# Kernel optimization log

Hardware: AMD Instinct MI355X
Metric: run time of the kernel (lower is better)

The kernel has to match this reference:

```python
import jax, jax.numpy as jnp
import numpy as np

B, S, D, H = 4, 2048, 1024, 16
DK = D // H


def setup_inputs() -> dict:
    key = jax.random.key(0)
    ks = jax.random.split(key, 5)
    init_std = np.sqrt(2.0 / (D + D))  # trunc bound proxy; plain randn clamped below
    trunc = 3 * init_std

    def w(k):
        return jnp.clip(jax.random.normal(k, (D, D), dtype=jnp.float32), -trunc, trunc)

    x = jax.random.normal(ks[0], (B, S, D), dtype=jnp.float32)
    return {
        "x": x,
        "W_Q": w(ks[1]),
        "W_K": w(ks[2]),
        "W_V": w(ks[3]),
        "W_O": w(ks[4]),
        "is_causal": 1,
    }


def reference(x, W_Q, W_K, W_V, W_O, is_causal):
    b, s, d = x.shape
    # Linear: y = W @ x with W:[out,in], x:[..., in]
    def proj(W, t):
        y = jnp.einsum("oi,bsi->bso", W, t)
        # [b, s, h*dk] -> [b, h, s, dk]
        return y.reshape(b, s, H, DK).transpose(0, 2, 1, 3)

    q = proj(W_Q, x)
    k = proj(W_K, x)
    v = proj(W_V, x)

    scores = jnp.einsum("bhqd,bhkd->bhqk", q, k) * (DK ** -0.5)
    if is_causal:
        causal = jnp.tril(jnp.ones((s, s), dtype=bool))
        scores = jnp.where(causal, scores, -jnp.inf)
    attn = jax.nn.softmax(scores, axis=-1)
    out = jnp.einsum("bhqk,bhkd->bhqd", attn, v)
    out = out.transpose(0, 2, 1, 3).reshape(b, s, H * DK)
    return jnp.einsum("oi,bsi->bso", W_O, out)
```

## Files before the change

kernel.cpp:

```cpp
#include <hip/hip_runtime.h>
#include <stdint.h>

#define NB 4
#define NS 2048
#define ND 1024
#define NH 16
#define NDK 64
#define L2E 1.44269504088896340736f
#define AS1 __attribute__((address_space(1)))
#define AS3 __attribute__((address_space(3)))

typedef __attribute__((ext_vector_type(8)))  short     s16x8;
typedef __attribute__((ext_vector_type(4)))  float     f32x4;
typedef __attribute__((ext_vector_type(16))) float     f32x16;
typedef __attribute__((ext_vector_type(4)))  unsigned  u32x4;

__device__ __forceinline__ unsigned short f2bf(float f) {
    union { float f; unsigned u; } v; v.f = f;
    unsigned r = v.u + 0x7FFFu + ((v.u >> 16) & 1u);
    return (unsigned short)(r >> 16);
}
__device__ __forceinline__ unsigned cvt_pk_bf16(float lo, float hi) {
    unsigned r;
    asm("v_cvt_pk_bf16_f32 %0, %1, %2" : "=v"(r) : "v"(lo), "v"(hi));
    return r;
}
__device__ __forceinline__ void pl32swap(unsigned &a, unsigned &b) {
    asm volatile("v_permlane32_swap_b32 %0, %1" : "+v"(a), "+v"(b));
}
__device__ __forceinline__ float exp2_hw(float x) {
    float r; asm("v_exp_f32 %0, %1" : "=v"(r) : "v"(x)); return r;
}
__device__ __forceinline__ f32x16 fz16() {
    f32x16 z;
#pragma unroll
    for (int r = 0; r < 16; ++r) z[r] = 0.f;
    return z;
}
__device__ __forceinline__ f32x16 mfma32(const s16x8& a, const s16x8& b, const f32x16& c) {
    return __builtin_amdgcn_mfma_f32_32x32x16_bf16(a, b, c, 0, 0, 0);
}

__global__ void detect_dtype(const unsigned* __restrict__ x, int* __restrict__ flag) {
    int lane = threadIdx.x;
    int cnt = 0;
    for (int i = lane; i < 1024; i += 64) {
        unsigned lo = x[i] & 0xFFFFu;
        unsigned e  = (lo >> 7) & 0xFFu;
        cnt += (e >= 100u && e <= 140u) ? 1 : 0;
    }
    for (int d = 1; d < 64; d <<= 1) cnt += __shfl_xor(cnt, d);
    if (lane == 0) flag[0] = (cnt > 512) ? 1 : 0;
}

__global__ void convert_bf16(const void* __restrict__ src, unsigned short* __restrict__ dst,
                             int n8, const int* __restrict__ flagp) {
    int i = blockIdx.x * blockDim.x + threadIdx.x;
    int stride = gridDim.x * blockDim.x;
    int fl = *flagp;
    for (; i < n8; i += stride) {
        u32x4 v;
        if (fl) {
            v = *(const u32x4*)((const unsigned short*)src + (long)i * 8);
        } else {
            const float* p = (const float*)src + (long)i * 8;
            f32x4 a = *(const f32x4*)p;
            f32x4 b = *(const f32x4*)(p + 4);
            v[0] = cvt_pk_bf16(a[0], a[1]);
            v[1] = cvt_pk_bf16(a[2], a[3]);
            v[2] = cvt_pk_bf16(b[0], b[1]);
            v[3] = cvt_pk_bf16(b[2], b[3]);
        }
        *(u32x4*)(dst + (long)i * 8) = v;
    }
}

__device__ __forceinline__ void stage_glds64(const unsigned short* __restrict__ src, int ld,
                                             long r0, int k0, unsigned short* lds, int tid) {
#pragma unroll
    for (int h = 0; h < 4; ++h) {
        int c = h * 256 + tid;
        int row = c >> 3;
        int scol = (c & 7) ^ (row & 7);
        const unsigned short* gp = src + (r0 + row) * ld + k0 + scol * 8;
        unsigned short* lp = lds + (c & ~63) * 8;
        __builtin_amdgcn_global_load_lds(
            (const AS1 unsigned short*)gp, (AS3 unsigned short*)lp, 16, 0, 0);
    }
}
__device__ __forceinline__ void stage_orig64(unsigned short* lds, const void* __restrict__ src,
                                             int ld, long r0, int k0, int fl, int tid) {
    if (fl) { stage_glds64((const unsigned short*)src, ld, r0, k0, lds, tid); return; }
#pragma unroll
    for (int h = 0; h < 4; ++h) {
        int c = h * 256 + tid;
        int row = c >> 3;
        int scol = (c & 7) ^ (row & 7);
        const float* p = (const float*)src + (r0 + row) * (long)ld + k0 + scol * 8;
        f32x4 a = *(const f32x4*)p;
        f32x4 b = *(const f32x4*)(p + 4);
        u32x4 v;
        v[0] = cvt_pk_bf16(a[0], a[1]);
        v[1] = cvt_pk_bf16(a[2], a[3]);
        v[2] = cvt_pk_bf16(b[0], b[1]);
        v[3] = cvt_pk_bf16(b[2], b[3]);
        *(u32x4*)(lds + c * 8) = v;
    }
}

template<int OUT_MODE, int A_ORIG, int B_ORIG, int GXL>
__global__ __launch_bounds__(256, 2)
void gemm3(const void* __restrict__ A, const void* __restrict__ W,
           void* __restrict__ dst, const int* __restrict__ flagp, float scale)
{
    __shared__ unsigned short As[128 * 64];
    __shared__ unsigned short Bs[128 * 64];
    const long TOKc = (long)NB * NS * ND;
    int tid  = threadIdx.x;
    int w    = tid >> 6, lane = tid & 63;
    int wr   = w >> 1,   wc   = w & 1;
    int nwg = (int)(gridDim.x * gridDim.y);
    int bid = (int)(blockIdx.y * gridDim.x + blockIdx.x);
    int nb  = (bid & 7) * (nwg >> 3) + (bid >> 3);
    int n0  = (nb & ((1 << GXL) - 1)) * 128;
    long m0 = (long)(nb >> GXL) * 128;
    int fl  = *flagp;

    f32x4 zero4 = {0.f, 0.f, 0.f, 0.f};
    f32x4 acc[4][4];
#pragma unroll
    for (int i = 0; i < 4; ++i)
#pragma unroll
        for (int j = 0; j < 4; ++j) acc[i][j] = zero4;

    int lr = lane & 15, lg = lane >> 4;

    for (int k0 = 0; k0 < 1024; k0 += 64) {
        __syncthreads();
        if (A_ORIG) stage_orig64(As, A, 1024, m0, k0, fl, tid);
        else        stage_glds64((const unsigned short*)A, 1024, m0, k0, As, tid);
        if (B_ORIG) stage_orig64(Bs, W, 1024, n0, k0, fl, tid);
        else        stage_glds64((const unsigned short*)W, 1024, n0, k0, Bs, tid);
        __syncthreads();
#pragma unroll
        for (int kk = 0; kk < 2; ++kk) {
            s16x8 af[4], bf[4];
#pragma unroll
            for (int i = 0; i < 4; ++i) {
                int row = wr * 64 + i * 16 + lr;
                int u = (kk * 4 + lg) ^ (lr & 7);
                af[i] = *(const s16x8*)(As + row * 64 + u * 8);
            }
#pragma unroll
            for (int j = 0; j < 4; ++j) {
                int row = wc * 64 + j * 16 + lr;
                int u = (kk * 4 + lg) ^ (lr & 7);
                bf[j] = *(const s16x8*)(Bs + row * 64 + u * 8);
            }
#pragma unroll
            for (int i = 0; i < 4; ++i)
#pragma unroll
                for (int j = 0; j < 4; ++j)
                    acc[i][j] = __builtin_amdgcn_mfma_f32_16x16x32_bf16(af[i], bf[j], acc[i][j], 0, 0, 0);
        }
    }

    int rbase = (lane >> 4) * 4;
#pragma unroll
    for (int i = 0; i < 4; ++i)
#pragma unroll
        for (int j = 0; j < 4; ++j)
#pragma unroll
            for (int r = 0; r < 4; ++r) {
                long m = m0 + wr * 64 + i * 16 + rbase + r;
                int  n = n0 + wc * 64 + j * 16 + lr;
                float v = acc[i][j][r];
                if (OUT_MODE == 0 || OUT_MODE == 3) {
                    long b = m >> 11, s = m & 2047;
                    int hh = (n >> 6) & 15, dk = n & 63;
                    float sc = (OUT_MODE == 0 || n < 1024) ? scale : 1.0f;
                    long off = (OUT_MODE == 3 && n >= 1024) ? TOKc : 0;
                    ((unsigned short*)dst)[off + (((b * NH + hh) * NS) + s) * NDK + dk] = f2bf(v * sc);
                } else if (OUT_MODE == 1) {
                    int hh = (int)(m >> 6), dk = (int)(m & 63);
                    long b = n >> 11, s = n & 2047;
                    ((unsigned short*)dst)[(((b * NH + hh) * NDK) + dk) * NS + s] = f2bf(v * scale);
                } else {
                    if (fl) ((unsigned short*)dst)[m * 1024 + n] = f2bf(v * scale);
                    else    ((float*)dst)[m * 1024 + n] = v * scale;
                }
            }
}

__device__ __forceinline__ void stage_tile64(const char* __restrict__ srcbase, int rowstride,
                                             unsigned short* lds, int tid) {
#pragma unroll
    for (int h = 0; h < 2; ++h) {
        int c = h * 256 + tid;
        int L = c * 16;
        int row = L >> 7;
        int sr  = (L & 127) ^ ((row & 7) << 4);
        const char* gp = srcbase + row * rowstride + sr;
        unsigned short* lp = lds + (c & ~63) * 8;
        __builtin_amdgcn_global_load_lds((const AS1 unsigned short*)gp,
                                         (AS3 unsigned short*)lp, 16, 0, 0);
    }
}

__device__ __forceinline__ void sm64s(f32x16& st0, f32x16& st1, float& l,
                                      bool mask, int kv0, int qb, int l31, int hi,
                                      s16x8* pf)
{
    if (mask) {
        int q = qb + l31;
#pragma unroll
        for (int r = 0; r < 16; ++r) {
            int crow = (r & 3) + 8 * (r >> 2) + 4 * hi;
            if (kv0 + crow > q)      st0[r] = -1e30f;
            if (kv0 + 32 + crow > q) st1[r] = -1e30f;
        }
    }
#pragma unroll
    for (int r = 0; r < 16; ++r) {
        st0[r] = exp2_hw(st0[r]);
        st1[r] = exp2_hw(st1[r]);
    }
    float s8[8];
#pragma unroll
    for (int r = 0; r < 8; ++r) s8[r] = (st0[r] + st0[r + 8]) + (st1[r] + st1[r + 8]);
    float s4[4];
#pragma unroll
    for (int r = 0; r < 4; ++r) s4[r] = s8[r] + s8[r + 4];
    l += (s4[0] + s4[1]) + (s4[2] + s4[3]);

#pragma unroll
    for (int half = 0; half < 2; ++half) {
        const f32x16& st = half ? st1 : st0;
        unsigned b0 = cvt_pk_bf16(st[0],  st[1]);
        unsigned b1 = cvt_pk_bf16(st[2],  st[3]);
        unsigned b2 = cvt_pk_bf16(st[4],  st[5]);
        unsigned b3 = cvt_pk_bf16(st[6],  st[7]);
        unsigned b4 = cvt_pk_bf16(st[8],  st[9]);
        unsigned b5 = cvt_pk_bf16(st[10], st[11]);
        unsigned b6 = cvt_pk_bf16(st[12], st[13]);
        unsigned b7 = cvt_pk_bf16(st[14], st[15]);
        pl32swap(b0, b2);  pl32swap(b1, b3);
        pl32swap(b4, b6);  pl32swap(b5, b7);
        union { unsigned u[4]; s16x8 v; } p0, p1;
        p0.u[0] = b0; p0.u[1] = b1; p0.u[2] = b2; p0.u[3] = b3;
        p1.u[0] = b4; p1.u[1] = b5; p1.u[2] = b6; p1.u[3] = b7;
        pf[half * 2]     = p0.v;
        pf[half * 2 + 1] = p1.v;
    }
}

__device__ __forceinline__ void attn_epi(unsigned short* epb, const f32x16& o0, const f32x16& o1,
                                         float lrow, int l31, int hi, int lane,
                                         unsigned short* __restrict__ Oo, int qb, int b, int hh)
{
    float lt = lrow + __shfl_xor(lrow, 32);
    float inv = 1.0f / lt;
#pragma unroll
    for (int j = 0; j < 2; ++j) {
        const f32x16& o = j ? o1 : o0;
#pragma unroll
        for (int g = 0; g < 4; ++g) {
            int d0 = j * 32 + g * 8 + hi * 4;
            unsigned lo = cvt_pk_bf16(o[g * 4 + 0] * inv, o[g * 4 + 1] * inv);
            unsigned hw = cvt_pk_bf16(o[g * 4 + 2] * inv, o[g * 4 + 3] * inv);
            unsigned short* p = epb + l31 * 72 + d0;
            *(unsigned*)(p)     = lo;
            *(unsigned*)(p + 2) = hw;
        }
    }
    asm volatile("s_waitcnt lgkmcnt(0)" ::: "memory");
    __builtin_amdgcn_sched_barrier(0);
#pragma unroll
    for (int rr = 0; rr < 4; ++rr) {
        int q2 = rr * 8 + (lane >> 3);
        int d2 = (lane & 7) * 8;
        u32x4 vv = *(const u32x4*)(epb + q2 * 72 + d2);
        *(u32x4*)(Oo + (((long)b * NS + qb + q2) * ND) + hh * NDK + d2) = vv;
    }
}

__global__ __launch_bounds__(256, 3)
void attn_fwd9(const unsigned short* __restrict__ Q,
               const unsigned short* __restrict__ Kt,
               const unsigned short* __restrict__ Vt,
               unsigned short* __restrict__ Oo,
               const int* __restrict__ causalp)
{
    __shared__ char lds[2][16384];
    int tid = threadIdx.x, w = tid >> 6, lane = tid & 63;
    int l31 = lane & 31, hi = lane >> 5;
    int bh = blockIdx.x;
    int j  = 15 - (int)blockIdx.y;
    int t  = 4 * j + w, qb = t * 32;
    int causal = *causalp;
    int nst   = causal ? (2 * j + 2) : (NS / 64);
    int sdiag = causal ? (t >> 1) : 0x7FFFFFFF;

    const unsigned short* Qh = Q  + bh * (NS * NDK);
    const char* Khb = (const char*)(Kt + (long)bh * NS * NDK);
    const char* Vhb = (const char*)(Vt + (long)bh * NDK * NS);

    s16x8 qf[4];
#pragma unroll
    for (int kd = 0; kd < 4; ++kd)
        qf[kd] = *(const s16x8*)(Qh + (qb + l31) * NDK + kd * 16 + hi * 8);

    int koff[4];
#pragma unroll
    for (int kd = 0; kd < 4; ++kd)
        koff[kd] = l31 * 128 + ((kd * 32 + hi * 16) ^ ((l31 & 7) << 4));

    const f32x16 Z16 = fz16();
    f32x16 o0 = fz16(), o1 = fz16();
    float l = 0.f;

    stage_tile64(Khb, 128, (unsigned short*)&lds[0][0], tid);
    stage_tile64(Vhb, NS * 2, (unsigned short*)&lds[0][8192], tid);
    __syncthreads();

    int cur = 0;
    for (int s = 0; s < nst; ++s) {
        if (s + 1 < nst) {
            int kv1 = (s + 1) * 64;
            stage_tile64(Khb + (long)kv1 * 128, 128, (unsigned short*)&lds[cur ^ 1][0], tid);
            stage_tile64(Vhb + kv1 * 2, NS * 2, (unsigned short*)&lds[cur ^ 1][8192], tid);
        }
        if (s <= sdiag) {
            const char* kb = &lds[cur][0];
            const char* vb = &lds[cur][8192];
            f32x16 st0, st1;
            {
                s16x8 k0 = *(const s16x8*)(kb + koff[0]);
                s16x8 k1 = *(const s16x8*)(kb + 4096 + koff[0]);
                st0 = mfma32(k0, qf[0], Z16);
                st1 = mfma32(k1, qf[0], Z16);
            }
#pragma unroll
            for (int kd = 1; kd < 4; ++kd) {
                s16x8 k0 = *(const s16x8*)(kb + koff[kd]);
                s16x8 k1 = *(const s16x8*)(kb + 4096 + koff[kd]);
                st0 = mfma32(k0, qf[kd], st0);
                st1 = mfma32(k1, qf[kd], st1);
            }
            s16x8 pf[4];
            sm64s(st0, st1, l, s == sdiag, s * 64, qb, l31, hi, pf);
#pragma unroll
            for (int ks = 0; ks < 4; ++ks) {
                s16x8 va = *(const s16x8*)(vb + koff[ks]);
                s16x8 wb = *(const s16x8*)(vb + 4096 + koff[ks]);
                o0 = mfma32(va, pf[ks], o0);
                o1 = mfma32(wb, pf[ks], o1);
            }
        }
        __syncthreads();
        cur ^= 1;
    }

    unsigned short* ep = (unsigned short*)&lds[0][0] + w * (32 * 72);
    attn_epi(ep, o0, o1, l, l31, hi, lane, Oo, qb, bh >> 4, bh & 15);
}

extern "C" void kernel_launch(void* const* d_in, const int* in_sizes, int n_in,
                              void* d_out, int out_size, void* d_ws, size_t ws_size,
                              hipStream_t stream) {
    const void* x  = d_in[0];
    const void* Wq = d_in[1];
    const void* Wk = d_in[2];
    const void* Wv = d_in[3];
    const void* Wo = d_in[4];
    const int* causal = (const int*)d_in[5];

    const long TOK  = (long)NB * NS * ND;
    const long WTOK = (long)ND * ND;
    size_t need = 256 + 4UL * TOK * 2;
    if (ws_size < need) return;

    char* ws = (char*)d_ws;
    int* flag = (int*)ws;
    unsigned short* Qb = (unsigned short*)(ws + 256);
    unsigned short* Kb = Qb + TOK;
    unsigned short* Vb = Kb + TOK;
    unsigned short* XB = Vb + TOK;
    unsigned short* Ab = XB;
    unsigned short* WQK = Vb + TOK - 2 * WTOK;
    unsigned short* WOB = Qb;

    detect_dtype<<<1, 64, 0, stream>>>((const unsigned*)x, flag);

    convert_bf16<<<2048, 256, 0, stream>>>(x,  XB,         (int)(TOK / 8),  flag);
    convert_bf16<<<512,  256, 0, stream>>>(Wq, WQK,        (int)(WTOK / 8), flag);
    convert_bf16<<<512,  256, 0, stream>>>(Wk, WQK + WTOK, (int)(WTOK / 8), flag);

    dim3 blk(256);
    gemm3<3, 0, 0, 4><<<dim3(16, 64), blk, 0, stream>>>(XB, WQK, Qb, flag, 0.125f * L2E);
    gemm3<1, 1, 0, 6><<<dim3(64, 8), blk, 0, stream>>>(Wv, XB, Vb, flag, 1.0f);
    attn_fwd9<<<dim3(64, 16), blk, 0, stream>>>(Qb, Kb, Vb, Ab, causal);
    convert_bf16<<<512, 256, 0, stream>>>(Wo, WOB, (int)(WTOK / 8), flag);
    gemm3<2, 0, 0, 3><<<dim3(8, 64), blk, 0, stream>>>(Ab, WOB, d_out, flag, 1.0f);
}
```

Measured before the change: 168.2 us.

## Balance causal attention tiles and pre-convert all QKV weights in one kernel

Merges the x, W_Q, W_K and W_V bf16 conversions into a single launch and stages W_V into scratch space at the tail of the output buffer. The V-projection GEMM then loads pre-converted bf16 through direct global-to-LDS loads instead of converting fp32 on the fly. The attention kernel now pairs a short and a long query tile per block (tiles 2j+w and 62-2j+w), so every block does a similar amount of causal work. The scratch area in d_out relies on the final GEMM overwriting it later, and the bf16-input path through the old stage_orig code has been removed.

```diff
diff --git a/kernel.cpp b/kernel.cpp
--- a/kernel.cpp
+++ b/kernel.cpp
@@ -51,6 +51,41 @@
     }
     for (int d = 1; d < 64; d <<= 1) cnt += __shfl_xor(cnt, d);
     if (lane == 0) flag[0] = (cnt > 512) ? 1 : 0;
+}
+
+__global__ void convert_all(const void* __restrict__ x,  const void* __restrict__ wq,
+                            const void* __restrict__ wk, const void* __restrict__ wv,
+                            unsigned short* __restrict__ XB, unsigned short* __restrict__ WQKV,
+                            const int* __restrict__ flagp) {
+    const int A  = (NB * NS * ND) / 8;
+    const int WC = (ND * ND) / 8;
+    int fl = *flagp;
+    int i = blockIdx.x * blockDim.x + threadIdx.x;
+    int stride = gridDim.x * blockDim.x;
+    int total = A + 3 * WC;
+    for (; i < total; i += stride) {
+        const void* src; unsigned short* dst; long o8;
+        if (i < A) { src = x; dst = XB; o8 = i; }
+        else {
+            int k = i - A, which = k >> 17, o = k & (WC - 1);
+            src = which == 0 ? wq : (which == 1 ? wk : wv);
+            dst = WQKV + (long)which * (ND * ND);
+            o8 = o;
+        }
+        u32x4 v;
+        if (fl) {
+            v = *(const u32x4*)((const unsigned short*)src + o8 * 8);
+        } else {
+            const float* p = (const float*)src + o8 * 8;
+            f32x4 a = *(const f32x4*)p;
+            f32x4 b = *(const f32x4*)(p + 4);
+            v[0] = cvt_pk_bf16(a[0], a[1]);
+            v[1] = cvt_pk_bf16(a[2], a[3]);
+            v[2] = cvt_pk_bf16(b[0], b[1]);
+            v[3] = cvt_pk_bf16(b[2], b[3]);
+        }
+        *(u32x4*)(dst + o8 * 8) = v;
+    }
 }
 
 __global__ void convert_bf16(const void* __restrict__ src, unsigned short* __restrict__ dst,
@@ -88,29 +123,10 @@
             (const AS1 unsigned short*)gp, (AS3 unsigned short*)lp, 16, 0, 0);
     }
 }
-__device__ __forceinline__ void stage_orig64(unsigned short* lds, const void* __restrict__ src,
-                                             int ld, long r0, int k0, int fl, int tid) {
-    if (fl) { stage_glds64((const unsigned short*)src, ld, r0, k0, lds, tid); return; }
-#pragma unroll
-    for (int h = 0; h < 4; ++h) {
-        int c = h * 256 + tid;
-        int row = c >> 3;
-        int scol = (c & 7) ^ (row & 7);
-        const float* p = (const float*)src + (r0 + row) * (long)ld + k0 + scol * 8;
-        f32x4 a = *(const f32x4*)p;
-        f32x4 b = *(const f32x4*)(p + 4);
-        u32x4 v;
-        v[0] = cvt_pk_bf16(a[0], a[1]);
-        v[1] = cvt_pk_bf16(a[2], a[3]);
-        v[2] = cvt_pk_bf16(b[0], b[1]);
-        v[3] = cvt_pk_bf16(b[2], b[3]);
-        *(u32x4*)(lds + c * 8) = v;
-    }
-}
-
-template<int OUT_MODE, int A_ORIG, int B_ORIG, int GXL>
+
+template<int OUT_MODE, int NXB>
 __global__ __launch_bounds__(256, 2)
-void gemm3(const void* __restrict__ A, const void* __restrict__ W,
+void gemm3(const unsigned short* __restrict__ A, const unsigned short* __restrict__ W,
            void* __restrict__ dst, const int* __restrict__ flagp, float scale)
 {
     __shared__ unsigned short As[128 * 64];
@@ -122,8 +138,8 @@
     int nwg = (int)(gridDim.x * gridDim.y);
     int bid = (int)(blockIdx.y * gridDim.x + blockIdx.x);
     int nb  = (bid & 7) * (nwg >> 3) + (bid >> 3);
-    int n0  = (nb & ((1 << GXL) - 1)) * 128;
-    long m0 = (long)(nb >> GXL) * 128;
+    int n0  = (nb % NXB) * 128;
+    long m0 = (long)(nb / NXB) * 128;
     int fl  = *flagp;
 
     f32x4 zero4 = {0.f, 0.f, 0.f, 0.f};
@@ -137,10 +153,8 @@
 
     for (int k0 = 0; k0 < 1024; k0 += 64) {
         __syncthreads();
-        if (A_ORIG) stage_orig64(As, A, 1024, m0, k0, fl, tid);
-        else        stage_glds64((const unsigned short*)A, 1024, m0, k0, As, tid);
-        if (B_ORIG) stage_orig64(Bs, W, 1024, n0, k0, fl, tid);
-        else        stage_glds64((const unsigned short*)W, 1024, n0, k0, Bs, tid);
+        stage_glds64(A, 1024, m0, k0, As, tid);
+        stage_glds64(W, 1024, n0, k0, Bs, tid);
         __syncthreads();
 #pragma unroll
         for (int kk = 0; kk < 2; ++kk) {
@@ -175,11 +189,11 @@
                 long m = m0 + wr * 64 + i * 16 + rbase + r;
                 int  n = n0 + wc * 64 + j * 16 + lr;
                 float v = acc[i][j][r];
-                if (OUT_MODE == 0 || OUT_MODE == 3) {
+                if (OUT_MODE == 3) {
                     long b = m >> 11, s = m & 2047;
                     int hh = (n >> 6) & 15, dk = n & 63;
-                    float sc = (OUT_MODE == 0 || n < 1024) ? scale : 1.0f;
-                    long off = (OUT_MODE == 3 && n >= 1024) ? TOKc : 0;
+                    float sc = (n < 1024) ? scale : 1.0f;
+                    long off = (n >= 1024) ? TOKc : 0;
                     ((unsigned short*)dst)[off + (((b * NH + hh) * NS) + s) * NDK + dk] = f2bf(v * sc);
                 } else if (OUT_MODE == 1) {
                     int hh = (int)(m >> 6), dk = (int)(m & 63);
@@ -285,20 +299,21 @@
 }
 
 __global__ __launch_bounds__(256, 3)
-void attn_fwd9(const unsigned short* __restrict__ Q,
-               const unsigned short* __restrict__ Kt,
-               const unsigned short* __restrict__ Vt,
-               unsigned short* __restrict__ Oo,
-               const int* __restrict__ causalp)
+void attn_fwd10(const unsigned short* __restrict__ Q,
+                const unsigned short* __restrict__ Kt,
+                const unsigned short* __restrict__ Vt,
+                unsigned short* __restrict__ Oo,
+                const int* __restrict__ causalp)
 {
     __shared__ char lds[2][16384];
     int tid = threadIdx.x, w = tid >> 6, lane = tid & 63;
     int l31 = lane & 31, hi = lane >> 5;
     int bh = blockIdx.x;
-    int j  = 15 - (int)blockIdx.y;
-    int t  = 4 * j + w, qb = t * 32;
+    int j  = blockIdx.y;
+    int t  = (w < 2) ? (2 * j + w) : (62 - 2 * j + (w & 1));
+    int qb = t * 32;
     int causal = *causalp;
-    int nst   = causal ? (2 * j + 2) : (NS / 64);
+    int nst   = causal ? (32 - j) : (NS / 64);
     int sdiag = causal ? (t >> 1) : 0x7FFFFFFF;
 
     const unsigned short* Qh = Q  + bh * (NS * NDK);
@@ -387,19 +402,16 @@
     unsigned short* Vb = Kb + TOK;
     unsigned short* XB = Vb + TOK;
     unsigned short* Ab = XB;
-    unsigned short* WQK = Vb + TOK - 2 * WTOK;
     unsigned short* WOB = Qb;
+    unsigned short* WQKV = (unsigned short*)((char*)d_out + (size_t)out_size * 2 - 3UL * WTOK * 2);
 
     detect_dtype<<<1, 64, 0, stream>>>((const unsigned*)x, flag);
-
-    convert_bf16<<<2048, 256, 0, stream>>>(x,  XB,         (int)(TOK / 8),  flag);
-    convert_bf16<<<512,  256, 0, stream>>>(Wq, WQK,        (int)(WTOK / 8), flag);
-    convert_bf16<<<512,  256, 0, stream>>>(Wk, WQK + WTOK, (int)(WTOK / 8), flag);
+    convert_all<<<2048, 256, 0, stream>>>(x, Wq, Wk, Wv, XB, WQKV, flag);
 
     dim3 blk(256);
-    gemm3<3, 0, 0, 4><<<dim3(16, 64), blk, 0, stream>>>(XB, WQK, Qb, flag, 0.125f * L2E);
-    gemm3<1, 1, 0, 6><<<dim3(64, 8), blk, 0, stream>>>(Wv, XB, Vb, flag, 1.0f);
-    attn_fwd9<<<dim3(64, 16), blk, 0, stream>>>(Qb, Kb, Vb, Ab, causal);
+    gemm3<3, 16><<<dim3(16, 64), blk, 0, stream>>>(XB, WQKV, Qb, flag, 0.125f * L2E);
+    gemm3<1, 64><<<dim3(64, 8), blk, 0, stream>>>(WQKV + 2 * WTOK, XB, Vb, flag, 1.0f);
+    attn_fwd10<<<dim3(64, 16), blk, 0, stream>>>(Qb, Kb, Vb, Ab, causal);
     convert_bf16<<<512, 256, 0, stream>>>(Wo, WOB, (int)(WTOK / 8), flag);
-    gemm3<2, 0, 0, 3><<<dim3(8, 64), blk, 0, stream>>>(Ab, WOB, d_out, flag, 1.0f);
-}
+    gemm3<2, 8><<<dim3(8, 64), blk, 0, stream>>>(Ab, WOB, d_out, flag, 1.0f);
+}
```

New measurement: 161.5 us. 1.04x faster.
